# Kernel optimization log

Measured on AMD Instinct MI355X. Metric: run time of the kernel, lower is better.

## Reference

```python
import jax, jax.numpy as jnp
import numpy as np

DIM = 4096
N_HEADS = 32
HEAD_DIM = DIM // N_HEADS  # 128
BSZ = 2
SEQLEN = 2048


def setup_inputs() -> dict:
    key = jax.random.key(0)
    ks = jax.random.split(key, 8)
    x = jax.random.normal(ks[0], (BSZ, SEQLEN, DIM), dtype=jnp.float32)
    # rotary frequencies (LLaMA): theta = 10000^{-2i/d}, angle = pos * theta
    inv_freq = 1.0 / (10000.0 ** (np.arange(0, HEAD_DIM, 2, dtype=np.float32) / HEAD_DIM))
    angles = np.arange(SEQLEN, dtype=np.float32)[:, None] * inv_freq[None, :]  # [S, hd/2]
    freqs_cos = jnp.asarray(np.cos(angles))
    freqs_sin = jnp.asarray(np.sin(angles))
    # causal additive mask [1,1,S,S]
    neg = jnp.float32(-1e9)
    mask = jnp.where(jnp.tril(jnp.ones((SEQLEN, SEQLEN), dtype=bool)), 0.0, neg)[None, None]
    scale = 0.02
    wq = jax.random.normal(ks[1], (DIM, DIM), dtype=jnp.float32) * scale
    wk = jax.random.normal(ks[2], (DIM, DIM), dtype=jnp.float32) * scale
    wv = jax.random.normal(ks[3], (DIM, DIM), dtype=jnp.float32) * scale
    wo = jax.random.normal(ks[4], (DIM, DIM), dtype=jnp.float32) * scale
    return {"x": x, "start_pos": 0, "freqs_cos": freqs_cos, "freqs_sin": freqs_sin,
            "mask": mask, "wq": wq, "wk": wk, "wv": wv, "wo": wo}


def _apply_rotary(t, cos, sin):
    # t: [B,S,H,hd]; cos/sin: [S,hd/2] -> broadcast [1,S,1,hd/2]
    t = t.reshape(*t.shape[:-1], HEAD_DIM // 2, 2)
    t0, t1 = t[..., 0], t[..., 1]
    c = cos[None, :, None, :]
    s = sin[None, :, None, :]
    r0 = t0 * c - t1 * s
    r1 = t0 * s + t1 * c
    return jnp.stack([r0, r1], axis=-1).reshape(*t0.shape[:-1], HEAD_DIM)


def reference(x, start_pos, freqs_cos, freqs_sin, mask, wq, wk, wv, wo):
    bsz, seqlen, _ = x.shape
    # QKV projections (nn.Linear: y = x @ W.T; weights stored [out,in])
    xq = (x @ wq.T).reshape(bsz, seqlen, N_HEADS, HEAD_DIM)
    xk = (x @ wk.T).reshape(bsz, seqlen, N_HEADS, HEAD_DIM)
    xv = (x @ wv.T).reshape(bsz, seqlen, N_HEADS, HEAD_DIM)
    xq = _apply_rotary(xq, freqs_cos, freqs_sin)
    xk = _apply_rotary(xk, freqs_cos, freqs_sin)
    # [B,H,S,hd]
    q = xq.transpose(0, 2, 1, 3)
    k = xk.transpose(0, 2, 1, 3)
    v = xv.transpose(0, 2, 1, 3)
    scale = 1.0 / jnp.sqrt(jnp.float32(HEAD_DIM))
    scores = jnp.einsum('bhqd,bhkd->bhqk', q, k) * scale + mask
    probs = jax.nn.softmax(scores, axis=-1)
    out = jnp.einsum('bhqk,bhkd->bhqd', probs, v)  # [B,H,S,hd]
    out = out.transpose(0, 2, 1, 3).reshape(bsz, seqlen, DIM)
    return out @ wo.T
```

## Files before the change

### kernel.cpp

```cpp
#include <hip/hip_runtime.h>

typedef unsigned short ushort_t;
typedef unsigned int u32;
typedef short bf16x8 __attribute__((ext_vector_type(8)));
typedef float f32x4 __attribute__((ext_vector_type(4)));
typedef float f32x16 __attribute__((ext_vector_type(16)));
typedef u32 u32x4 __attribute__((ext_vector_type(4)));

__device__ __forceinline__ ushort_t f2bf(float f) {
  u32 u = __builtin_bit_cast(u32, f);
  u += 0x7FFFu + ((u >> 16) & 1u);
  return (ushort_t)(u >> 16);
}
__device__ __forceinline__ float bf2f(u32 bits16) {
  return __builtin_bit_cast(float, bits16 << 16);
}

__device__ __forceinline__ void cvt_body(const float* __restrict__ in,
                                         ushort_t* __restrict__ out, int i) {
  const float4 a = ((const float4*)in)[(size_t)i * 2];
  const float4 b = ((const float4*)in)[(size_t)i * 2 + 1];
  uint4 r;
  r.x = (u32)f2bf(a.x) | ((u32)f2bf(a.y) << 16);
  r.y = (u32)f2bf(a.z) | ((u32)f2bf(a.w) << 16);
  r.z = (u32)f2bf(b.x) | ((u32)f2bf(b.y) << 16);
  r.w = (u32)f2bf(b.z) | ((u32)f2bf(b.w) << 16);
  ((uint4*)out)[i] = r;
}

__device__ __forceinline__ void cvt_perm_body(const float* __restrict__ in,
                                              ushort_t* __restrict__ out, int i) {
  const int row = i >> 9, k8 = i & 511;
  const int q = row & 31;
  const int lrow = (row & ~31) | ((q < 16) ? (2 * q) : (2 * (q - 16) + 1));
  const float4 a = ((const float4*)in)[(size_t)lrow * 1024 + k8 * 2];
  const float4 b = ((const float4*)in)[(size_t)lrow * 1024 + k8 * 2 + 1];
  uint4 r;
  r.x = (u32)f2bf(a.x) | ((u32)f2bf(a.y) << 16);
  r.y = (u32)f2bf(a.z) | ((u32)f2bf(a.w) << 16);
  r.z = (u32)f2bf(b.x) | ((u32)f2bf(b.y) << 16);
  r.w = (u32)f2bf(b.z) | ((u32)f2bf(b.w) << 16);
  ((uint4*)out)[(size_t)row * 512 + k8] = r;
}

__global__ __launch_bounds__(256)
void cvt_kernel(const float* __restrict__ in, ushort_t* __restrict__ out) {
  cvt_body(in, out, blockIdx.x * 256 + threadIdx.x);
}

__global__ __launch_bounds__(256)
void cvt_perm_kernel(const float* __restrict__ in, ushort_t* __restrict__ out) {
  cvt_perm_body(in, out, blockIdx.x * 256 + threadIdx.x);
}

__global__ __launch_bounds__(256)
void cvt2_kernel(const float* __restrict__ i0, ushort_t* __restrict__ o0,
                 const float* __restrict__ i1, ushort_t* __restrict__ o1,
                 const float* __restrict__ fcos, const float* __restrict__ fsin,
                 float2* __restrict__ cst) {
  const int i = blockIdx.x * 256 + threadIdx.x;
  if (blockIdx.y == 0) {
    if (blockIdx.x < 512) cst[i] = make_float2(fcos[i], fsin[i]);
    cvt_body(i0, o0, i);
  } else {
    cvt_perm_body(i1, o1, i);
  }
}

template <int F32OUT, int ROPE>
__global__ __launch_bounds__(512, 2)
void gemm256(const ushort_t* __restrict__ A, const ushort_t* __restrict__ B,
             void* __restrict__ C, const float2* __restrict__ cst, float qsc) {
  constexpr int KD = 4096, ND = 4096;
  __shared__ ushort_t sA[2][2][128 * 64];
  __shared__ ushort_t sB[2][2][128 * 64];
  const int tid = threadIdx.x;
  const int lane = tid & 63, wave = tid >> 6;
  const int lq = lane & 15, g = lane >> 4;
  const int wm = wave >> 2, wn = wave & 3;
  const int id = blockIdx.x;
  const int swz = (id & 7) * 32 + (id >> 3);
  const int bm = (swz >> 4) * 256;
  const int bn = (swz & 15) * 256;
  const int csw = ((lane & 7) ^ (lane >> 3)) * 8;
  const int srow = lane >> 3;

  f32x4 acc[8][4];
#pragma unroll
  for (int m = 0; m < 8; ++m)
#pragma unroll
    for (int n = 0; n < 4; ++n) acc[m][n] = (f32x4)0.f;

#define STG(sbuf, G, rowb, t_, s_, h_)                                               \
  {                                                                                  \
    _Pragma("unroll") for (int i_ = 0; i_ < 2; ++i_) {                               \
      const int r0_ = wave * 16 + i_ * 8;                                            \
      const int tc_ = (t_) > 63 ? 63 : (t_);                                         \
      const ushort_t* src_ =                                                         \
          (G) + (size_t)((rowb) + (h_) * 128 + r0_ + srow) * KD + tc_ * 64 + csw;    \
      __builtin_amdgcn_global_load_lds(                                              \
          (const __attribute__((address_space(1))) u32*)src_,                        \
          (__attribute__((address_space(3))) u32*)&sbuf[s_][h_][r0_ * 64 + lane * 8],\
          16, 0, 0);                                                                 \
    }                                                                                \
  }
#define RD_A(S_, H_, mf_, kk_)                                                        \
  (*(const bf16x8*)&sA[S_][H_][(wm * 64 + (mf_) * 16 + lq) * 64 +                     \
                               ((((kk_) * 4 + g) ^ (lq & 7)) * 8)])
#define RD_B(S_, H_, nf_, kk_)                                                        \
  (*(const bf16x8*)&sB[S_][H_][(wn * 32 + (nf_) * 16 + lq) * 64 +                     \
                               ((((kk_) * 4 + g) ^ (lq & 7)) * 8)])
#define MMQ(MB, NB, BR)                                                               \
  _Pragma("unroll") for (int mf = 0; mf < 4; ++mf)                                    \
    _Pragma("unroll") for (int nf = 0; nf < 2; ++nf)                                  \
      _Pragma("unroll") for (int kk = 0; kk < 2; ++kk)                                \
        acc[(MB) + mf][(NB) + nf] = __builtin_amdgcn_mfma_f32_16x16x32_bf16(          \
            af[mf][kk], BR[nf][kk], acc[(MB) + mf][(NB) + nf], 0, 0, 0)

  STG(sA, A, bm, 0, 0, 0); STG(sA, A, bm, 0, 0, 1);
  STG(sB, B, bn, 0, 0, 0); STG(sB, B, bn, 0, 0, 1);
  STG(sA, A, bm, 1, 1, 0); STG(sA, A, bm, 1, 1, 1);
  STG(sB, B, bn, 1, 1, 1);
  asm volatile("s_waitcnt vmcnt(6)" ::: "memory");
  __builtin_amdgcn_s_barrier();

  bf16x8 af[4][2], b0[2][2], b1[2][2];

#define TILE(S_, T_)                                                                  \
                      \
  _Pragma("unroll") for (int mf = 0; mf < 4; ++mf)                                    \
    _Pragma("unroll") for (int kk = 0; kk < 2; ++kk)                                  \
      af[mf][kk] = RD_A(S_, 0, mf, kk);                                               \
  _Pragma("unroll") for (int nf = 0; nf < 2; ++nf)                                    \
    _Pragma("unroll") for (int kk = 0; kk < 2; ++kk)                                  \
      b0[nf][kk] = RD_B(S_, 0, nf, kk);                                               \
  STG(sB, B, bn, (T_) + 1, (S_) ^ 1, 0);                                              \
  __builtin_amdgcn_s_barrier();                                                       \
  __builtin_amdgcn_s_setprio(1);                                                      \
  MMQ(0, 0, b0);                                                                      \
  __builtin_amdgcn_s_setprio(0);                                                      \
  __builtin_amdgcn_s_barrier();                                                       \
                                                \
  _Pragma("unroll") for (int nf = 0; nf < 2; ++nf)                                    \
    _Pragma("unroll") for (int kk = 0; kk < 2; ++kk)                                  \
      b1[nf][kk] = RD_B(S_, 1, nf, kk);                                               \
  __builtin_amdgcn_s_barrier();                                                       \
  __builtin_amdgcn_s_setprio(1);                                                      \
  MMQ(0, 2, b1);                                                                      \
  __builtin_amdgcn_s_setprio(0);                                                      \
  __builtin_amdgcn_s_barrier();                                                       \
                              \
  _Pragma("unroll") for (int mf = 0; mf < 4; ++mf)                                    \
    _Pragma("unroll") for (int kk = 0; kk < 2; ++kk)                                  \
      af[mf][kk] = RD_A(S_, 1, mf, kk);                                               \
  STG(sA, A, bm, (T_) + 2, S_, 0);                                                    \
  __builtin_amdgcn_s_barrier();                                                       \
  __builtin_amdgcn_s_setprio(1);                                                      \
  MMQ(4, 2, b1);                                                                      \
  __builtin_amdgcn_s_setprio(0);                                                      \
  __builtin_amdgcn_s_barrier();                                                       \
                     \
  STG(sA, A, bm, (T_) + 2, S_, 1);                                                    \
  STG(sB, B, bn, (T_) + 2, S_, 1);                                                    \
  asm volatile("s_waitcnt vmcnt(6)" ::: "memory");                                    \
  __builtin_amdgcn_s_barrier();                                                       \
  __builtin_amdgcn_s_setprio(1);                                                      \
  MMQ(4, 0, b0);                                                                      \
  __builtin_amdgcn_s_setprio(0);                                                      \
  __builtin_amdgcn_s_barrier();

  for (int t = 0; t < 64; t += 2) {
    TILE(0, t)
    TILE(1, t + 1)
  }
#undef TILE
#undef STG
#undef RD_A
#undef RD_B
#undef MMQ

  if (ROPE) {
    const int p = wn * 16 + lq;
#pragma unroll
    for (int m = 0; m < 8; ++m) {
      const int grow = bm + (m >> 2) * 128 + wm * 64 + (m & 3) * 16 + g * 4;
#pragma unroll
      for (int r = 0; r < 4; ++r) {
        const int row = grow + r;
        const float2 cs = cst[(size_t)(row & 2047) * 64 + p];
#pragma unroll
        for (int pr = 0; pr < 2; ++pr) {
          const float t0 = acc[m][pr * 2][r];
          const float t1 = acc[m][pr * 2 + 1][r];
          const int c0 = bn + pr * 128 + wn * 32 + lq;
          ((ushort_t*)C)[(size_t)row * ND + c0] =
              f2bf((t0 * cs.x - t1 * cs.y) * qsc);
          ((ushort_t*)C)[(size_t)row * ND + c0 + 16] =
              f2bf((t0 * cs.y + t1 * cs.x) * qsc);
        }
      }
    }
  } else {
#pragma unroll
    for (int m = 0; m < 8; ++m) {
      const int grow = bm + (m >> 2) * 128 + wm * 64 + (m & 3) * 16 + g * 4;
#pragma unroll
      for (int r = 0; r < 4; ++r) {
        const int row = grow + r;
#pragma unroll
        for (int n = 0; n < 4; ++n) {
          const int gcol = bn + (n >> 1) * 128 + wn * 32 + (n & 1) * 16 + lq;
          if (F32OUT)
            ((float*)C)[(size_t)row * ND + gcol] = acc[m][n][r];
          else
            ((ushort_t*)C)[(size_t)row * ND + gcol] = f2bf(acc[m][n][r]);
        }
      }
    }
  }
}

__global__ __launch_bounds__(256, 2)
void attn_kernel(const ushort_t* __restrict__ Q, const ushort_t* __restrict__ K,
                 const ushort_t* __restrict__ Vt, ushort_t* __restrict__ O) {
  __shared__ ushort_t sK[2][32 * 128];
  __shared__ ushort_t sV[2][128 * 32];
  __shared__ float sScr[4][32];

  const int lane = threadIdx.x & 63, wave = threadIdx.x >> 6;
  const int lq = lane & 31, hi = lane >> 5;
  const int bp = blockIdx.x;
  const int bh = bp >> 3, j = bp & 7;
  const int h = bh & 31, b = bh >> 5;
  const ushort_t* Kb_ = K + (size_t)(b * 2048) * 4096 + h * 128;
  const ushort_t* Vb_ = Vt + (size_t)(h * 128) * 4096 + b * 2048;

#define STAGE(buf, kt_)                                                              \
  {                                                                                  \
    const int kb_ = (kt_) * 32;                                                      \
    _Pragma("unroll")                                                                \
    for (int i_ = 0; i_ < 2; ++i_) {                                                 \
      const int c_ = wave + i_ * 4;                                                  \
      const int krow = c_ * 4 + (lane >> 4);                                         \
      const int kcol = (lane & 15) ^ (krow & 7);                                     \
      const ushort_t* ksrc = Kb_ + (size_t)(kb_ + krow) * 4096 + kcol * 8;           \
      __builtin_amdgcn_global_load_lds(                                              \
          (const __attribute__((address_space(1))) u32*)ksrc,                        \
          (__attribute__((address_space(3))) u32*)&sK[buf][c_ * 512 + lane * 8],     \
          16, 0, 0);                                                                 \
      const int sst = c_ * 64 + lane;                                                \
      const int dv = sst >> 2;                                                       \
      const int gl = (sst & 3) ^ ((sst >> 3) & 3);                                   \
      const ushort_t* vsrc = Vb_ + (size_t)dv * 4096 + kb_ + gl * 8;                 \
      __builtin_amdgcn_global_load_lds(                                              \
          (const __attribute__((address_space(1))) u32*)vsrc,                        \
          (__attribute__((address_space(3))) u32*)&sV[buf][sst * 8], 16, 0, 0);      \
    }                                                                                \
  }

  for (int ph = 0; ph < 2; ++ph) {
    const int qj = ph ? (15 - j) : j;
    const int qbase = qj * 128 + wave * 32;
    const int ntw = qj * 4 + wave + 1;
    const int ntmax = qj * 4 + 4;

    bf16x8 aq[8];
    const ushort_t* qrow = Q + (size_t)(b * 2048 + qbase + lq) * 4096 + h * 128 + hi * 8;
#pragma unroll
    for (int kf = 0; kf < 8; ++kf) aq[kf] = *(const bf16x8*)(qrow + kf * 16);

    f32x16 o[4];
#pragma unroll
    for (int dt = 0; dt < 4; ++dt) o[dt] = (f32x16)0.f;
    float m_run = -1e30f, l_run = 0.f;

    int cur = 0;
    STAGE(0, 0);
    __syncthreads();

    for (int kt = 0; kt < ntmax; ++kt) {
      if (kt + 1 < ntmax) STAGE(cur ^ 1, kt + 1);
      if (kt < ntw) {
        const int kb = kt * 32;
        f32x16 st = (f32x16)0.f;
#pragma unroll
        for (int kf = 0; kf < 8; ++kf) {
          const bf16x8 kfrag =
              *(const bf16x8*)&sK[cur][lq * 128 + (((kf * 2 + hi) ^ (lq & 7)) * 8)];
          st = __builtin_amdgcn_mfma_f32_32x32x16_bf16(kfrag, aq[kf], st, 0, 0, 0);
        }
        if (kt == ntw - 1) {
          const int q = qbase + lq;
#pragma unroll
          for (int r = 0; r < 16; ++r) {
            const int key = kb + (r & 3) + 8 * (r >> 2) + 4 * hi;
            if (key > q) st[r] = -1e30f;
          }
        }
        float tm = st[0];
#pragma unroll
        for (int r = 1; r < 16; ++r) tm = fmaxf(tm, st[r]);
        tm = fmaxf(tm, __shfl_xor(tm, 32));
        if (!__all(tm <= m_run + 8.f)) {
          const float mnew = fmaxf(m_run, tm);
          const float corr = __expf(m_run - mnew);
          m_run = mnew;
          l_run *= corr;
          if (hi == 0) sScr[wave][lq] = corr;
          float fr[16];
#pragma unroll
          for (int r = 0; r < 16; ++r)
            fr[r] = sScr[wave][(r & 3) + 8 * (r >> 2) + 4 * hi];
#pragma unroll
          for (int dt = 0; dt < 4; ++dt)
#pragma unroll
            for (int r = 0; r < 16; ++r) o[dt][r] *= fr[r];
        }
        float rs = 0.f;
#pragma unroll
        for (int r = 0; r < 16; ++r) { st[r] = __expf(st[r] - m_run); rs += st[r]; }
        rs += __shfl_xor(rs, 32);
        l_run += rs;
        u32 A_, B_, C_, D_, E_, F_, G_, H_;
#define CVTPK(d_, l_, h_) \
  asm("v_cvt_pk_bf16_f32 %0, %1, %2" : "=v"(d_) : "v"(l_), "v"(h_))
        CVTPK(A_, st[0], st[1]);  CVTPK(B_, st[4], st[5]);
        CVTPK(C_, st[2], st[3]);  CVTPK(D_, st[6], st[7]);
        CVTPK(E_, st[8], st[9]);  CVTPK(F_, st[12], st[13]);
        CVTPK(G_, st[10], st[11]); CVTPK(H_, st[14], st[15]);
#undef CVTPK
        asm volatile("v_permlane32_swap_b32 %0, %1" : "+v"(A_), "+v"(B_));
        asm volatile("v_permlane32_swap_b32 %0, %1" : "+v"(C_), "+v"(D_));
        asm volatile("v_permlane32_swap_b32 %0, %1" : "+v"(E_), "+v"(F_));
        asm volatile("v_permlane32_swap_b32 %0, %1" : "+v"(G_), "+v"(H_));
        const bf16x8 pa0 = __builtin_bit_cast(bf16x8, (u32x4){A_, C_, B_, D_});
        const bf16x8 pa1 = __builtin_bit_cast(bf16x8, (u32x4){E_, G_, F_, H_});
#pragma unroll
        for (int dt = 0; dt < 4; ++dt) {
          const int d0 = dt * 32 + lq;
          const int s0 = 4 * d0 + ((hi + 0) ^ ((d0 >> 1) & 3));
          const int s1 = 4 * d0 + ((hi + 2) ^ ((d0 >> 1) & 3));
          const bf16x8 vf0 = *(const bf16x8*)&sV[cur][s0 * 8];
          const bf16x8 vf1 = *(const bf16x8*)&sV[cur][s1 * 8];
          o[dt] = __builtin_amdgcn_mfma_f32_32x32x16_bf16(pa0, vf0, o[dt], 0, 0, 0);
          o[dt] = __builtin_amdgcn_mfma_f32_32x32x16_bf16(pa1, vf1, o[dt], 0, 0, 0);
        }
      }
      __syncthreads();
      cur ^= 1;
    }

    if (hi == 0) sScr[wave][lq] = 1.f / l_run;
    __syncthreads();
    const size_t obase = (size_t)(b * 2048 + qbase) * 4096 + h * 128;
#pragma unroll
    for (int r = 0; r < 16; ++r) {
      const int qr = (r & 3) + 8 * (r >> 2) + 4 * hi;
      const float f = sScr[wave][qr];
#pragma unroll
      for (int dt = 0; dt < 4; ++dt)
        O[obase + (size_t)qr * 4096 + dt * 32 + lq] = f2bf(o[dt][r] * f);
    }
    __syncthreads();
  }
#undef STAGE
}

extern "C" void kernel_launch(void* const* d_in, const int* in_sizes, int n_in,
                              void* d_out, int out_size, void* d_ws, size_t ws_size,
                              hipStream_t stream) {
  const float* x = (const float*)d_in[0];
  const float* fcos = (const float*)d_in[2];
  const float* fsin = (const float*)d_in[3];
  const float* wq = (const float*)d_in[5];
  const float* wk = (const float*)d_in[6];
  const float* wv = (const float*)d_in[7];
  const float* wo = (const float*)d_in[8];
  float* out = (float*)d_out;
  char* ws = (char*)d_ws;
  const size_t MB32 = 33554432;
  ushort_t* xb = (ushort_t*)(ws);
  ushort_t* wb = (ushort_t*)(ws + MB32);
  ushort_t* Qb = (ushort_t*)(ws + 2 * MB32);
  ushort_t* Kb = (ushort_t*)(ws + 3 * MB32);
  ushort_t* Vt = (ushort_t*)(ws + 4 * MB32);
  ushort_t* Ob = xb;
  float2* cst = (float2*)d_out;

  const dim3 cb(256);
  const dim3 cg(8192);
  const dim3 gb(512);
  const dim3 gg(256);
  const float QSC = 0.08838834764831845f;

  hipLaunchKernelGGL(cvt2_kernel, dim3(8192, 2), cb, 0, stream, x, xb, wq, wb,
                     fcos, fsin, cst);
  hipLaunchKernelGGL((gemm256<0, 1>), gg, gb, 0, stream, xb, wb, (void*)Qb, cst, QSC);
  hipLaunchKernelGGL(cvt_perm_kernel, cg, cb, 0, stream, wk, wb);
  hipLaunchKernelGGL((gemm256<0, 1>), gg, gb, 0, stream, xb, wb, (void*)Kb, cst, 1.f);
  hipLaunchKernelGGL(cvt_kernel, cg, cb, 0, stream, wv, wb);
  hipLaunchKernelGGL((gemm256<0, 0>), gg, gb, 0, stream, wb, xb, (void*)Vt, cst, 1.f);
  hipLaunchKernelGGL(attn_kernel, dim3(512), cb, 0, stream, Qb, Kb, Vt, Ob);
  hipLaunchKernelGGL(cvt_kernel, cg, cb, 0, stream, wo, wb);
  hipLaunchKernelGGL((gemm256<1, 0>), gg, gb, 0, stream, Ob, wb, (void*)out, cst, 1.f);
}
```

Before: 677.2 us.

## Overlap weight conversions with GEMM and attention via extra blocks; tune LDS waits

The standalone fp32-to-bf16 weight conversion kernels are removed. Their work now runs in extra thread blocks appended to the preceding GEMM or attention launch, so conversion overlaps compute, and buffers are ping-ponged (the Vt region temporarily holds converted wk). The GEMM inner loop also gains explicit lgkmcnt waits around barriers. This cuts launch count and idle tails, at the cost of sharing CUs with the compute blocks and tighter buffer-reuse ordering.

```diff
diff --git a/kernel.cpp b/kernel.cpp
--- a/kernel.cpp
+++ b/kernel.cpp
@@ -44,16 +44,6 @@
 }
 
 __global__ __launch_bounds__(256)
-void cvt_kernel(const float* __restrict__ in, ushort_t* __restrict__ out) {
-  cvt_body(in, out, blockIdx.x * 256 + threadIdx.x);
-}
-
-__global__ __launch_bounds__(256)
-void cvt_perm_kernel(const float* __restrict__ in, ushort_t* __restrict__ out) {
-  cvt_perm_body(in, out, blockIdx.x * 256 + threadIdx.x);
-}
-
-__global__ __launch_bounds__(256)
 void cvt2_kernel(const float* __restrict__ i0, ushort_t* __restrict__ o0,
                  const float* __restrict__ i1, ushort_t* __restrict__ o1,
                  const float* __restrict__ fcos, const float* __restrict__ fsin,
@@ -67,18 +57,29 @@
   }
 }
 
-template <int F32OUT, int ROPE>
+template <int F32OUT, int ROPE, int CVT>
 __global__ __launch_bounds__(512, 2)
 void gemm256(const ushort_t* __restrict__ A, const ushort_t* __restrict__ B,
-             void* __restrict__ C, const float2* __restrict__ cst, float qsc) {
+             void* __restrict__ C, const float2* __restrict__ cst, float qsc,
+             const float* __restrict__ csrc, ushort_t* __restrict__ cdst) {
   constexpr int KD = 4096, ND = 4096;
   __shared__ ushort_t sA[2][2][128 * 64];
   __shared__ ushort_t sB[2][2][128 * 64];
   const int tid = threadIdx.x;
+  const int id = blockIdx.x;
+  if (CVT && id >= 256) {
+    const int cb_ = id - 256;
+#pragma unroll 2
+    for (int it = 0; it < 8; ++it) {
+      const int i = it * 262144 + cb_ * 512 + tid;
+      if (CVT == 1) cvt_perm_body(csrc, cdst, i);
+      else cvt_body(csrc, cdst, i);
+    }
+    return;
+  }
   const int lane = tid & 63, wave = tid >> 6;
   const int lq = lane & 15, g = lane >> 4;
   const int wm = wave >> 2, wn = wave & 3;
-  const int id = blockIdx.x;
   const int swz = (id & 7) * 32 + (id >> 3);
   const int bm = (swz >> 4) * 256;
   const int bn = (swz & 15) * 256;
@@ -135,7 +136,9 @@
     _Pragma("unroll") for (int kk = 0; kk < 2; ++kk)                                  \
       b0[nf][kk] = RD_B(S_, 0, nf, kk);                                               \
   STG(sB, B, bn, (T_) + 1, (S_) ^ 1, 0);                                              \
-  __builtin_amdgcn_s_barrier();                                                       \
+  asm volatile("s_waitcnt lgkmcnt(8)" ::: "memory");                                  \
+  __builtin_amdgcn_s_barrier();                                                       \
+  asm volatile("s_waitcnt lgkmcnt(0)" ::: "memory");                                  \
   __builtin_amdgcn_s_setprio(1);                                                      \
   MMQ(0, 0, b0);                                                                      \
   __builtin_amdgcn_s_setprio(0);                                                      \
@@ -145,6 +148,7 @@
     _Pragma("unroll") for (int kk = 0; kk < 2; ++kk)                                  \
       b1[nf][kk] = RD_B(S_, 1, nf, kk);                                               \
   __builtin_amdgcn_s_barrier();                                                       \
+  asm volatile("s_waitcnt lgkmcnt(0)" ::: "memory");                                  \
   __builtin_amdgcn_s_setprio(1);                                                      \
   MMQ(0, 2, b1);                                                                      \
   __builtin_amdgcn_s_setprio(0);                                                      \
@@ -155,6 +159,7 @@
       af[mf][kk] = RD_A(S_, 1, mf, kk);                                               \
   STG(sA, A, bm, (T_) + 2, S_, 0);                                                    \
   __builtin_amdgcn_s_barrier();                                                       \
+  asm volatile("s_waitcnt lgkmcnt(0)" ::: "memory");                                  \
   __builtin_amdgcn_s_setprio(1);                                                      \
   MMQ(4, 2, b1);                                                                      \
   __builtin_amdgcn_s_setprio(0);                                                      \
@@ -222,14 +227,23 @@
 
 __global__ __launch_bounds__(256, 2)
 void attn_kernel(const ushort_t* __restrict__ Q, const ushort_t* __restrict__ K,
-                 const ushort_t* __restrict__ Vt, ushort_t* __restrict__ O) {
+                 const ushort_t* __restrict__ Vt, ushort_t* __restrict__ O,
+                 const float* __restrict__ csrc, ushort_t* __restrict__ cdst) {
   __shared__ ushort_t sK[2][32 * 128];
   __shared__ ushort_t sV[2][128 * 32];
   __shared__ float sScr[4][32];
 
+  const int bp = blockIdx.x;
+  if (bp >= 512) {
+    const int cb_ = bp - 512;
+#pragma unroll 2
+    for (int it = 0; it < 16; ++it)
+      cvt_body(csrc, cdst, it * 131072 + cb_ * 256 + threadIdx.x);
+    return;
+  }
+
   const int lane = threadIdx.x & 63, wave = threadIdx.x >> 6;
   const int lq = lane & 31, hi = lane >> 5;
-  const int bp = blockIdx.x;
   const int bh = bp >> 3, j = bp & 7;
   const int h = bh & 31, b = bh >> 5;
   const ushort_t* Kb_ = K + (size_t)(b * 2048) * 4096 + h * 128;
@@ -388,19 +402,18 @@
   float2* cst = (float2*)d_out;
 
   const dim3 cb(256);
-  const dim3 cg(8192);
   const dim3 gb(512);
-  const dim3 gg(256);
   const float QSC = 0.08838834764831845f;
 
   hipLaunchKernelGGL(cvt2_kernel, dim3(8192, 2), cb, 0, stream, x, xb, wq, wb,
                      fcos, fsin, cst);
-  hipLaunchKernelGGL((gemm256<0, 1>), gg, gb, 0, stream, xb, wb, (void*)Qb, cst, QSC);
-  hipLaunchKernelGGL(cvt_perm_kernel, cg, cb, 0, stream, wk, wb);
-  hipLaunchKernelGGL((gemm256<0, 1>), gg, gb, 0, stream, xb, wb, (void*)Kb, cst, 1.f);
-  hipLaunchKernelGGL(cvt_kernel, cg, cb, 0, stream, wv, wb);
-  hipLaunchKernelGGL((gemm256<0, 0>), gg, gb, 0, stream, wb, xb, (void*)Vt, cst, 1.f);
-  hipLaunchKernelGGL(attn_kernel, dim3(512), cb, 0, stream, Qb, Kb, Vt, Ob);
-  hipLaunchKernelGGL(cvt_kernel, cg, cb, 0, stream, wo, wb);
-  hipLaunchKernelGGL((gemm256<1, 0>), gg, gb, 0, stream, Ob, wb, (void*)out, cst, 1.f);
-}
+  hipLaunchKernelGGL((gemm256<0, 1, 1>), dim3(768), gb, 0, stream, xb, wb,
+                     (void*)Qb, cst, QSC, wk, Vt);
+  hipLaunchKernelGGL((gemm256<0, 1, 2>), dim3(768), gb, 0, stream, xb, Vt,
+                     (void*)Kb, cst, 1.f, wv, wb);
+  hipLaunchKernelGGL((gemm256<0, 0, 0>), dim3(256), gb, 0, stream, wb, xb,
+                     (void*)Vt, cst, 1.f, nullptr, nullptr);
+  hipLaunchKernelGGL(attn_kernel, dim3(1024), cb, 0, stream, Qb, Kb, Vt, Ob, wo, wb);
+  hipLaunchKernelGGL((gemm256<1, 0, 0>), dim3(256), gb, 0, stream, Ob, wb,
+                     (void*)out, cst, 1.f, nullptr, nullptr);
+}
```

After: 667.6 us. No clear change (-1.4%).
